# Optimization experiments

Measured on AMD Instinct MI355X. Metric: run time of the kernel, lower is better.

The kernel has to match this reference:

```python
import jax, jax.numpy as jnp
import numpy as np

EPS = 1e-6


def _clinear(xr, xi, wr, wi):
    # nn.Linear applies x @ W.T; complex multiply (xr+i*xi)(Wr+i*Wi)
    r = xr @ wr.T - xi @ wi.T
    im = xi @ wr.T + xr @ wi.T
    return r, im


def setup_inputs() -> dict:
    key = jax.random.key(0)
    ks = jax.random.split(key, 11)
    B, S, D = 16384, 16, 64
    return {
        "z_real": jax.random.normal(ks[0], (B, D), jnp.float32),
        "z_imag": jax.random.normal(ks[1], (B, D), jnp.float32),
        "mem": jax.random.normal(ks[2], (B, S, 2 * D), jnp.float32),
        "ptr": jax.random.uniform(ks[3], (B, S), jnp.float32),
        "ctrl": jax.random.normal(ks[4], (B, 3), jnp.float32),
        "w_q_real": jax.random.normal(ks[5], (D, D), jnp.float32),
        "w_q_imag": jax.random.normal(ks[6], (D, D), jnp.float32),
        "w_k_real": jax.random.normal(ks[7], (D, D), jnp.float32),
        "w_k_imag": jax.random.normal(ks[8], (D, D), jnp.float32),
        "w_v_real": jax.random.normal(ks[9], (D, D), jnp.float32),
        "w_v_imag": jax.random.normal(ks[10], (D, D), jnp.float32),
    }


def reference(z_real, z_imag, mem, ptr, ctrl,
              w_q_real, w_q_imag, w_k_real, w_k_imag, w_v_real, w_v_imag):
    D = z_real.shape[-1]
    scale = D ** (-0.5)

    # differentiable push/pop/stay gates
    g = jax.nn.sigmoid(ctrl)                      # [B, 3]
    total = g.sum(-1, keepdims=True) + EPS
    push = (g[:, 0:1] / total)                    # [B, 1]
    pop = (g[:, 1:2] / total)
    stay = (g[:, 2:3] / total)

    # pointer shifts (torch.roll semantics)
    ptr_up = jnp.roll(ptr, 1, axis=1)
    ptr_down = jnp.roll(ptr, -1, axis=1)
    new_ptr = push * ptr_up + pop * ptr_down + stay * ptr  # [B, S]

    # blended write of current state into every memory slot
    z_flat = jnp.concatenate([z_real, z_imag], axis=-1)    # [B, 2D]
    p = push[:, :, None]                                   # [B, 1, 1]
    mem_new = mem * (1.0 - p) + p * z_flat[:, None, :]     # [B, S, 2D]

    mr, mi = mem_new[..., :D], mem_new[..., D:]

    # complex attention over memory slots
    qr, qi = _clinear(mr, mi, w_q_real, w_q_imag)
    kr, ki = _clinear(mr, mi, w_k_real, w_k_imag)
    vr, vi = _clinear(mr, mi, w_v_real, w_v_imag)
    q_flat = jnp.concatenate([qr, qi], axis=-1)            # [B, S, 2D]
    k_flat = jnp.concatenate([kr, ki], axis=-1)
    scores = jnp.einsum('bsd,btd->bst', q_flat, k_flat) * scale
    attn = jax.nn.softmax(scores, axis=-1)                 # [B, S, S]
    ar = jnp.einsum('bst,btd->bsd', attn, vr)
    ai = jnp.einsum('bst,btd->bsd', attn, vi)
    attended_flat = jnp.concatenate([ar, ai], axis=-1)     # [B, S, 2D]

    # pointer-weighted read
    read_flat = (attended_flat * new_ptr[:, :, None]).sum(1)  # [B, 2D]
    z_read_real = read_flat[:, :D]
    z_read_imag = read_flat[:, D:]

    active_slots = (new_ptr > 0.1).astype(jnp.float32).sum(1).mean()
    return z_read_real, z_read_imag, mem_new, new_ptr, active_slots
```

## Files before the change

### kernel.cpp

```cpp
#include <hip/hip_runtime.h>
#include <math.h>

#define GRID  512
#define BLK   512
#define NB    4
#define NITER 8

typedef __attribute__((ext_vector_type(8))) short short8;
typedef __attribute__((ext_vector_type(4))) float f32x4;

__device__ __forceinline__ float sigf(float x) { return 1.0f / (1.0f + expf(-x)); }

__device__ __forceinline__ unsigned short f2bf(float x) {
    unsigned u = __float_as_uint(x);
    return (unsigned short)((u + 0x7fffu + ((u >> 16) & 1u)) >> 16);
}
__device__ __forceinline__ float bf2f(unsigned short h) {
    return __uint_as_float(((unsigned)h) << 16);
}
__device__ __forceinline__ unsigned short f2bf_trunc(float x) {
    return (unsigned short)(__float_as_uint(x) >> 16);
}

__device__ __forceinline__ void split8(const float4 p0, const float4 p1,
                                       short8& hi, short8& lo) {
    float xs[8] = {p0.x, p0.y, p0.z, p0.w, p1.x, p1.y, p1.z, p1.w};
#pragma unroll
    for (int i = 0; i < 8; ++i) {
        unsigned short h = f2bf(xs[i]);
        hi[i] = (short)h;
        lo[i] = (short)f2bf_trunc(xs[i] - bf2f(h));
    }
}

__device__ __forceinline__ float Mmat(const float* __restrict__ wr,
                                      const float* __restrict__ wi, int k, int j) {
    if (j < 64) return (k < 64) ? wr[j * 64 + k] : -wi[j * 64 + (k - 64)];
    return (k < 64) ? wi[(j - 64) * 64 + k] : wr[(j - 64) * 64 + (k - 64)];
}

__global__ void prep_kernel(const float* __restrict__ wqr, const float* __restrict__ wqi,
                            const float* __restrict__ wkr, const float* __restrict__ wki,
                            const float* __restrict__ wvr, const float* __restrict__ wvi,
                            float* __restrict__ G, float* __restrict__ Mv,
                            int* __restrict__ cnt) {
    const int a = blockIdx.x;
    const int bb = threadIdx.x;
    if (a == 0 && bb == 0) *cnt = 0;
    float acc = 0.f;
    for (int j = 0; j < 128; ++j)
        acc += Mmat(wqr, wqi, a, j) * Mmat(wkr, wki, bb, j);
    G[a * 128 + bb] = 0.125f * acc;
    Mv[a * 128 + bb] = Mmat(wvr, wvi, a, bb);
}

__global__ void prep_frag(const float* __restrict__ G, const float* __restrict__ Mv,
                          unsigned short* __restrict__ Gf, unsigned short* __restrict__ Mvf) {
    const int bid = blockIdx.x;
    const int lane = threadIdx.x;
    const int mat = bid >> 5, jt = (bid >> 2) & 7, t = bid & 3;
    const float* X = mat ? Mv : G;
    unsigned short* O = mat ? Mvf : Gf;
    const int quad = lane >> 4, col = lane & 15;
    const int obase = ((jt * 4 + t) * 2) * 512 + lane * 8;
#pragma unroll
    for (int i = 0; i < 8; ++i) {
        int k = t * 32 + quad * 8 + i;
        int j = jt * 16 + col;
        float x = X[k * 128 + j];
        unsigned short h = f2bf(x);
        O[obase + i] = h;
        O[obase + 512 + i] = f2bf_trunc(x - bf2f(h));
    }
}

__global__ __launch_bounds__(BLK, 4) void crsn_main(
    const float* __restrict__ z_real, const float* __restrict__ z_imag,
    const float* __restrict__ mem, const float* __restrict__ ptr,
    const float* __restrict__ ctrl,
    const unsigned short* __restrict__ Gf, const unsigned short* __restrict__ Mvf,
    float* __restrict__ o_zr, float* __restrict__ o_zi,
    float* __restrict__ o_mem, float* __restrict__ o_np,
    int* __restrict__ g_cnt) {
    __shared__ __align__(16) float buf[NB * 2112];
    __shared__ __align__(16) unsigned short mfrag[NB * 8 * 520];
    __shared__ float wl[NB][16];
    __shared__ int cnt_lds;

    const int tid = threadIdx.x;
    const int w = tid >> 6;
    const int lane = tid & 63;
    const int quad = lane >> 4;
    const int col = lane & 15;
    const int snb = w >> 1;
    const int half = w & 1;

    if (tid == 0) cnt_lds = 0;

    f32x4 acc1[NB], acc2[NB];

    for (int it = 0; it < NITER; ++it) {
        const int base = blockIdx.x * (NB * NITER) + it * NB;
        const int bs = base + snb;

        {
            const float* gsrc = mem + (size_t)bs * 2048 + half * 1024;
#pragma unroll
            for (int c = 0; c < 4; ++c) {
                __builtin_amdgcn_global_load_lds(
                    (const __attribute__((address_space(1))) unsigned int*)(gsrc + c * 256 + lane * 4),
                    (__attribute__((address_space(3))) unsigned int*)(&buf[snb * 2112 + half * 1024 + c * 256]),
                    16, 0, 0);
            }
        }
        float g0 = sigf(ctrl[bs * 3 + 0]);
        float g1 = sigf(ctrl[bs * 3 + 1]);
        float g2 = sigf(ctrl[bs * 3 + 2]);
        float push = g0 / (g0 + g1 + g2 + 1e-6f);
        float qq = 1.0f - push;

        __builtin_amdgcn_s_waitcnt(0x0f70);

#pragma unroll
        for (int c = 0; c < 4; ++c) {
            int fi = half * 256 + c * 64 + lane;
            int su = fi >> 5, k = (fi & 31) << 2;
            float4 m4 = *(const float4*)&buf[snb * 2112 + fi * 4];
            float4 z4 = (k < 64) ? *(const float4*)(z_real + (bs << 6) + k)
                                 : *(const float4*)(z_imag + (bs << 6) + k - 64);
            float4 mn;
            mn.x = m4.x * qq + push * z4.x;
            mn.y = m4.y * qq + push * z4.y;
            mn.z = m4.z * qq + push * z4.z;
            mn.w = m4.w * qq + push * z4.w;
            *(float4*)(o_mem + (size_t)bs * 2048 + fi * 4) = mn;
            int t = k >> 5, q2 = (k >> 3) & 3, i0 = k & 7;
            int bidx = ((snb * 4 + t) * 2) * 520 + (q2 * 16 + su) * 8 + i0;
            ushort4 hv, lv;
            hv.x = f2bf(mn.x); hv.y = f2bf(mn.y); hv.z = f2bf(mn.z); hv.w = f2bf(mn.w);
            lv.x = f2bf_trunc(mn.x - bf2f(hv.x));
            lv.y = f2bf_trunc(mn.y - bf2f(hv.y));
            lv.z = f2bf_trunc(mn.z - bf2f(hv.z));
            lv.w = f2bf_trunc(mn.w - bf2f(hv.w));
            *(ushort4*)&mfrag[bidx] = hv;
            *(ushort4*)&mfrag[bidx + 520] = lv;
        }
        __syncthreads();

        {
#pragma unroll
            for (int nb = 0; nb < NB; ++nb) {
                acc1[nb] = (f32x4){0.f, 0.f, 0.f, 0.f};
                acc2[nb] = (f32x4){0.f, 0.f, 0.f, 0.f};
            }
#pragma unroll
            for (int t = 0; t < 4; ++t) {
                const unsigned short* fb = Gf + ((w * 4 + t) * 2) * 512 + lane * 8;
                const unsigned short* fb2 = Mvf + ((w * 4 + t) * 2) * 512 + lane * 8;
                short8 Gh = *(const short8*)fb;
                short8 Gl = *(const short8*)(fb + 512);
                short8 Mh = *(const short8*)fb2;
                short8 Ml = *(const short8*)(fb2 + 512);
#pragma unroll
                for (int nb = 0; nb < NB; ++nb) {
                    const unsigned short* mp = &mfrag[((nb * 4 + t) * 2) * 520 + lane * 8];
                    short8 ah = *(const short8*)mp;
                    short8 al = *(const short8*)(mp + 520);
                    acc1[nb] = __builtin_amdgcn_mfma_f32_16x16x32_bf16(ah, Gh, acc1[nb], 0, 0, 0);
                    acc1[nb] = __builtin_amdgcn_mfma_f32_16x16x32_bf16(ah, Gl, acc1[nb], 0, 0, 0);
                    acc1[nb] = __builtin_amdgcn_mfma_f32_16x16x32_bf16(al, Gh, acc1[nb], 0, 0, 0);
                    acc2[nb] = __builtin_amdgcn_mfma_f32_16x16x32_bf16(ah, Mh, acc2[nb], 0, 0, 0);
                    acc2[nb] = __builtin_amdgcn_mfma_f32_16x16x32_bf16(ah, Ml, acc2[nb], 0, 0, 0);
                    acc2[nb] = __builtin_amdgcn_mfma_f32_16x16x32_bf16(al, Mh, acc2[nb], 0, 0, 0);
                }
            }
#pragma unroll
            for (int nb = 0; nb < NB; ++nb)
#pragma unroll
                for (int reg = 0; reg < 4; ++reg)
                    buf[nb * 2112 + (quad * 4 + reg) * 132 + w * 16 + col] = acc1[nb][reg];
        }
        __syncthreads();

        if (w < NB) {
            const int b2 = base + w;
            float h0 = sigf(ctrl[b2 * 3 + 0]);
            float h1 = sigf(ctrl[b2 * 3 + 1]);
            float h2 = sigf(ctrl[b2 * 3 + 2]);
            float ht = h0 + h1 + h2 + 1e-6f;
            float pushb = h0 / ht, popb = h1 / ht, stayb = h2 / ht;

            int s = lane & 15;
            float pv = ptr[(b2 << 4) + s];
            float up = ptr[(b2 << 4) + ((s + 15) & 15)];
            float dn = ptr[(b2 << 4) + ((s + 1) & 15)];
            float npv = pushb * up + popb * dn + stayb * pv;
            if (lane < 16) o_np[(b2 << 4) + lane] = npv;
            unsigned long long bal = __ballot(lane < 16 && npv > 0.1f);
            if (lane == 0) atomicAdd(&cnt_lds, (int)__popcll(bal));

            f32x4 sc = (f32x4){0.f, 0.f, 0.f, 0.f};
#pragma unroll
            for (int t = 0; t < 4; ++t) {
                const float* tp = &buf[w * 2112 + col * 132 + t * 32 + quad * 8];
                float4 p0 = *(const float4*)tp;
                float4 p1 = *(const float4*)(tp + 4);
                short8 ah, al;
                split8(p0, p1, ah, al);
                const unsigned short* mp = &mfrag[((w * 4 + t) * 2) * 520 + lane * 8];
                short8 bh = *(const short8*)mp;
                short8 bl = *(const short8*)(mp + 520);
                sc = __builtin_amdgcn_mfma_f32_16x16x32_bf16(ah, bh, sc, 0, 0, 0);
                sc = __builtin_amdgcn_mfma_f32_16x16x32_bf16(ah, bl, sc, 0, 0, 0);
                sc = __builtin_amdgcn_mfma_f32_16x16x32_bf16(al, bh, sc, 0, 0, 0);
            }
            float at[4];
#pragma unroll
            for (int reg = 0; reg < 4; ++reg) {
                float v = sc[reg];
                float mx = v;
                mx = fmaxf(mx, __shfl_xor(mx, 1));
                mx = fmaxf(mx, __shfl_xor(mx, 2));
                mx = fmaxf(mx, __shfl_xor(mx, 4));
                mx = fmaxf(mx, __shfl_xor(mx, 8));
                float e = expf(v - mx);
                float s2 = e;
                s2 += __shfl_xor(s2, 1);
                s2 += __shfl_xor(s2, 2);
                s2 += __shfl_xor(s2, 4);
                s2 += __shfl_xor(s2, 8);
                at[reg] = e / s2;
            }
            float wv = __shfl(npv, quad * 4 + 0) * at[0] + __shfl(npv, quad * 4 + 1) * at[1]
                     + __shfl(npv, quad * 4 + 2) * at[2] + __shfl(npv, quad * 4 + 3) * at[3];
            wv += __shfl_xor(wv, 16);
            wv += __shfl_xor(wv, 32);
            if (lane < 16) wl[w][lane] = wv;
        }
        __syncthreads();

#pragma unroll
        for (int nb = 0; nb < NB; ++nb) {
            float pr = wl[nb][quad * 4 + 0] * acc2[nb][0]
                     + wl[nb][quad * 4 + 1] * acc2[nb][1]
                     + wl[nb][quad * 4 + 2] * acc2[nb][2]
                     + wl[nb][quad * 4 + 3] * acc2[nb][3];
            pr += __shfl_xor(pr, 16);
            pr += __shfl_xor(pr, 32);
            if (lane < 16) {
                int j = (w << 4) + lane;
                int b2 = base + nb;
                if (j < 64) o_zr[(b2 << 6) + j] = pr;
                else        o_zi[(b2 << 6) + j - 64] = pr;
            }
        }
    }
    __syncthreads();
    if (tid == 0) atomicAdd(g_cnt, cnt_lds);
}

__global__ void fin_kernel(const int* __restrict__ cnt, float* __restrict__ o_act) {
    *o_act = (float)(*cnt) / 16384.0f;
}

extern "C" void kernel_launch(void* const* d_in, const int* in_sizes, int n_in,
                              void* d_out, int out_size, void* d_ws, size_t ws_size,
                              hipStream_t stream) {
    const float* z_real = (const float*)d_in[0];
    const float* z_imag = (const float*)d_in[1];
    const float* mem    = (const float*)d_in[2];
    const float* ptr    = (const float*)d_in[3];
    const float* ctrl   = (const float*)d_in[4];
    const float* wqr = (const float*)d_in[5];
    const float* wqi = (const float*)d_in[6];
    const float* wkr = (const float*)d_in[7];
    const float* wki = (const float*)d_in[8];
    const float* wvr = (const float*)d_in[9];
    const float* wvi = (const float*)d_in[10];

    float* out = (float*)d_out;
    float* o_zr  = out;
    float* o_zi  = out + 16384 * 64;
    float* o_mem = out + 2 * 16384 * 64;
    float* o_np  = o_mem + 16384 * 16 * 128;
    float* o_act = o_np + 16384 * 16;

    int*   cnt = (int*)d_ws;
    float* G   = (float*)((char*)d_ws + 256);
    float* Mv  = G + 128 * 128;
    unsigned short* Gfr  = (unsigned short*)(Mv + 128 * 128);
    unsigned short* Mvfr = Gfr + 32768;

    hipLaunchKernelGGL(prep_kernel, dim3(128), dim3(128), 0, stream,
                       wqr, wqi, wkr, wki, wvr, wvi, G, Mv, cnt);
    hipLaunchKernelGGL(prep_frag, dim3(64), dim3(64), 0, stream, G, Mv, Gfr, Mvfr);
    hipLaunchKernelGGL(crsn_main, dim3(GRID), dim3(BLK), 0, stream,
                       z_real, z_imag, mem, ptr, ctrl, Gfr, Mvfr,
                       o_zr, o_zi, o_mem, o_np, cnt);
    hipLaunchKernelGGL(fin_kernel, dim3(1), dim3(1), 0, stream, cnt, o_act);
}
```

Before: 373.1 us.

## Prefetch next iteration's mem, z, ctrl and ptr into registers with nontemporal loads

Replaces the per-iteration global_load_lds staging of the memory tile, and its immediate wait, with register prefetch of the next iteration's mem, z, ctrl and ptr data issued during the current iteration. The aim is to hide global load latency behind the MFMA and softmax work. It also switches the mem loads and o_mem stores to nontemporal, and gets the rolled ptr neighbours by lane shuffles instead of three global loads. The cost is more registers per thread, which at 512 threads with launch bounds 4 may cause spills or lower occupancy.

```diff
diff --git a/kernel.cpp b/kernel.cpp
--- a/kernel.cpp
+++ b/kernel.cpp
@@ -82,7 +82,7 @@
     float* __restrict__ o_zr, float* __restrict__ o_zi,
     float* __restrict__ o_mem, float* __restrict__ o_np,
     int* __restrict__ g_cnt) {
-    __shared__ __align__(16) float buf[NB * 2112];
+    __shared__ __align__(16) float t1s[NB * 2112];
     __shared__ __align__(16) unsigned short mfrag[NB * 8 * 520];
     __shared__ float wl[NB][16];
     __shared__ int cnt_lds;
@@ -94,56 +94,70 @@
     const int col = lane & 15;
     const int snb = w >> 1;
     const int half = w & 1;
+    const int l31 = lane & 31;
+    const int k0 = l31 << 2;
+    const int t0 = l31 >> 3;
+    const int q2 = (l31 >> 1) & 3;
+    const int i0 = (lane & 1) << 2;
 
     if (tid == 0) cnt_lds = 0;
 
     f32x4 acc1[NB], acc2[NB];
+
+    const int base0 = blockIdx.x * (NB * NITER);
+    f32x4 pm[4];
+    f32x4 pz;
+    float cb0, cb1, cb2;
+    float pva;
+    float ca0, ca1, ca2;
+    {
+        const int bs = base0 + snb;
+        const f32x4* msrc = (const f32x4*)mem + (size_t)bs * 512 + half * 256 + lane;
+#pragma unroll
+        for (int c = 0; c < 4; ++c) pm[c] = __builtin_nontemporal_load(msrc + c * 64);
+        pz = (l31 < 16) ? *(const f32x4*)(z_real + (bs << 6) + k0)
+                        : *(const f32x4*)(z_imag + (bs << 6) + k0 - 64);
+        cb0 = ctrl[bs * 3 + 0]; cb1 = ctrl[bs * 3 + 1]; cb2 = ctrl[bs * 3 + 2];
+        const int b2 = base0 + (w & 3);
+        pva = ptr[(b2 << 4) + col];
+        ca0 = ctrl[b2 * 3 + 0]; ca1 = ctrl[b2 * 3 + 1]; ca2 = ctrl[b2 * 3 + 2];
+    }
 
     for (int it = 0; it < NITER; ++it) {
         const int base = blockIdx.x * (NB * NITER) + it * NB;
+        const int nbase = (it + 1 < NITER) ? base + NB : base;
         const int bs = base + snb;
 
         {
-            const float* gsrc = mem + (size_t)bs * 2048 + half * 1024;
+            float g0 = sigf(cb0), g1 = sigf(cb1), g2 = sigf(cb2);
+            float push = g0 / (g0 + g1 + g2 + 1e-6f);
+            float qq = 1.0f - push;
+            f32x4* odst = (f32x4*)o_mem + (size_t)bs * 512 + half * 256 + lane;
 #pragma unroll
             for (int c = 0; c < 4; ++c) {
-                __builtin_amdgcn_global_load_lds(
-                    (const __attribute__((address_space(1))) unsigned int*)(gsrc + c * 256 + lane * 4),
-                    (__attribute__((address_space(3))) unsigned int*)(&buf[snb * 2112 + half * 1024 + c * 256]),
-                    16, 0, 0);
-            }
-        }
-        float g0 = sigf(ctrl[bs * 3 + 0]);
-        float g1 = sigf(ctrl[bs * 3 + 1]);
-        float g2 = sigf(ctrl[bs * 3 + 2]);
-        float push = g0 / (g0 + g1 + g2 + 1e-6f);
-        float qq = 1.0f - push;
-
-        __builtin_amdgcn_s_waitcnt(0x0f70);
-
-#pragma unroll
-        for (int c = 0; c < 4; ++c) {
-            int fi = half * 256 + c * 64 + lane;
-            int su = fi >> 5, k = (fi & 31) << 2;
-            float4 m4 = *(const float4*)&buf[snb * 2112 + fi * 4];
-            float4 z4 = (k < 64) ? *(const float4*)(z_real + (bs << 6) + k)
-                                 : *(const float4*)(z_imag + (bs << 6) + k - 64);
-            float4 mn;
-            mn.x = m4.x * qq + push * z4.x;
-            mn.y = m4.y * qq + push * z4.y;
-            mn.z = m4.z * qq + push * z4.z;
-            mn.w = m4.w * qq + push * z4.w;
-            *(float4*)(o_mem + (size_t)bs * 2048 + fi * 4) = mn;
-            int t = k >> 5, q2 = (k >> 3) & 3, i0 = k & 7;
-            int bidx = ((snb * 4 + t) * 2) * 520 + (q2 * 16 + su) * 8 + i0;
-            ushort4 hv, lv;
-            hv.x = f2bf(mn.x); hv.y = f2bf(mn.y); hv.z = f2bf(mn.z); hv.w = f2bf(mn.w);
-            lv.x = f2bf_trunc(mn.x - bf2f(hv.x));
-            lv.y = f2bf_trunc(mn.y - bf2f(hv.y));
-            lv.z = f2bf_trunc(mn.z - bf2f(hv.z));
-            lv.w = f2bf_trunc(mn.w - bf2f(hv.w));
-            *(ushort4*)&mfrag[bidx] = hv;
-            *(ushort4*)&mfrag[bidx + 520] = lv;
+                int su = half * 8 + c * 2 + (lane >> 5);
+                f32x4 mn = pm[c] * qq + pz * push;
+                __builtin_nontemporal_store(mn, odst + c * 64);
+                int bidx = ((snb * 4 + t0) * 2) * 520 + (q2 * 16 + su) * 8 + i0;
+                ushort4 hv, lv;
+                hv.x = f2bf(mn[0]); hv.y = f2bf(mn[1]);
+                hv.z = f2bf(mn[2]); hv.w = f2bf(mn[3]);
+                lv.x = f2bf_trunc(mn[0] - bf2f(hv.x));
+                lv.y = f2bf_trunc(mn[1] - bf2f(hv.y));
+                lv.z = f2bf_trunc(mn[2] - bf2f(hv.z));
+                lv.w = f2bf_trunc(mn[3] - bf2f(hv.w));
+                *(ushort4*)&mfrag[bidx] = hv;
+                *(ushort4*)&mfrag[bidx + 520] = lv;
+            }
+        }
+        {
+            const int bs2 = nbase + snb;
+            const f32x4* msrc = (const f32x4*)mem + (size_t)bs2 * 512 + half * 256 + lane;
+#pragma unroll
+            for (int c = 0; c < 4; ++c) pm[c] = __builtin_nontemporal_load(msrc + c * 64);
+            pz = (l31 < 16) ? *(const f32x4*)(z_real + (bs2 << 6) + k0)
+                            : *(const f32x4*)(z_imag + (bs2 << 6) + k0 - 64);
+            cb0 = ctrl[bs2 * 3 + 0]; cb1 = ctrl[bs2 * 3 + 1]; cb2 = ctrl[bs2 * 3 + 2];
         }
         __syncthreads();
 
@@ -178,23 +192,19 @@
             for (int nb = 0; nb < NB; ++nb)
 #pragma unroll
                 for (int reg = 0; reg < 4; ++reg)
-                    buf[nb * 2112 + (quad * 4 + reg) * 132 + w * 16 + col] = acc1[nb][reg];
+                    t1s[nb * 2112 + (quad * 4 + reg) * 132 + w * 16 + col] = acc1[nb][reg];
         }
         __syncthreads();
 
         if (w < NB) {
             const int b2 = base + w;
-            float h0 = sigf(ctrl[b2 * 3 + 0]);
-            float h1 = sigf(ctrl[b2 * 3 + 1]);
-            float h2 = sigf(ctrl[b2 * 3 + 2]);
+            float h0 = sigf(ca0), h1 = sigf(ca1), h2 = sigf(ca2);
             float ht = h0 + h1 + h2 + 1e-6f;
             float pushb = h0 / ht, popb = h1 / ht, stayb = h2 / ht;
 
-            int s = lane & 15;
-            float pv = ptr[(b2 << 4) + s];
-            float up = ptr[(b2 << 4) + ((s + 15) & 15)];
-            float dn = ptr[(b2 << 4) + ((s + 1) & 15)];
-            float npv = pushb * up + popb * dn + stayb * pv;
+            float up = __shfl(pva, (lane + 15) & 15);
+            float dn = __shfl(pva, (lane + 1) & 15);
+            float npv = pushb * up + popb * dn + stayb * pva;
             if (lane < 16) o_np[(b2 << 4) + lane] = npv;
             unsigned long long bal = __ballot(lane < 16 && npv > 0.1f);
             if (lane == 0) atomicAdd(&cnt_lds, (int)__popcll(bal));
@@ -202,7 +212,7 @@
             f32x4 sc = (f32x4){0.f, 0.f, 0.f, 0.f};
 #pragma unroll
             for (int t = 0; t < 4; ++t) {
-                const float* tp = &buf[w * 2112 + col * 132 + t * 32 + quad * 8];
+                const float* tp = &t1s[w * 2112 + col * 132 + t * 32 + quad * 8];
                 float4 p0 = *(const float4*)tp;
                 float4 p1 = *(const float4*)(tp + 4);
                 short8 ah, al;
@@ -237,6 +247,11 @@
             wv += __shfl_xor(wv, 32);
             if (lane < 16) wl[w][lane] = wv;
         }
+        {
+            const int b2n = nbase + (w & 3);
+            pva = ptr[(b2n << 4) + col];
+            ca0 = ctrl[b2n * 3 + 0]; ca1 = ctrl[b2n * 3 + 1]; ca2 = ctrl[b2n * 3 + 2];
+        }
         __syncthreads();
 
 #pragma unroll
```

Measured after the change: 420.1 us. +12.6%, slower.
